# Kernel optimization log

Measured on AMD Instinct MI355X. Metric: run time of the kernel, lower is better.

Reference implementation:

```python
import jax, jax.numpy as jnp
import numpy as np

B, N, DIM = 4, 2048, 1024
HEADS, DIM_HEAD = 16, 64
SCALE = DIM_HEAD ** -0.5


def setup_inputs() -> dict:
    key = jax.random.key(0)
    ks = jax.random.split(key, 5)
    x = jax.random.normal(ks[0], (B, N, DIM), dtype=jnp.float32)
    s = DIM ** -0.5
    Wq = jax.random.normal(ks[1], (DIM, HEADS * DIM_HEAD), dtype=jnp.float32) * s
    Wk = jax.random.normal(ks[2], (DIM, HEADS * DIM_HEAD), dtype=jnp.float32) * s
    Wv = jax.random.normal(ks[3], (DIM, HEADS * DIM_HEAD), dtype=jnp.float32) * s
    Wo = jax.random.normal(ks[4], (HEADS * DIM_HEAD, DIM), dtype=jnp.float32) * s
    bo = jnp.zeros((DIM,), dtype=jnp.float32)
    return {"x": x, "Wq": Wq, "Wk": Wk, "Wv": Wv, "Wo": Wo, "bo": bo}


def reference(x, Wq, Wk, Wv, Wo, bo):
    b, n, _ = x.shape
    # project and split heads: [b, n, h, d] -> [b, h, n, d]
    def split_heads(t):
        return t.reshape(b, n, HEADS, DIM_HEAD).transpose(0, 2, 1, 3)
    q = split_heads(x @ Wq)
    k = split_heads(x @ Wk)
    v = split_heads(x @ Wv)
    dots = jnp.einsum("bhid,bhjd->bhij", q, k) * SCALE  # [b,h,n,n]
    attn = jax.nn.softmax(dots, axis=-1)
    out = jnp.einsum("bhij,bhjd->bhid", attn, v)  # [b,h,n,d]
    out = out.transpose(0, 2, 1, 3).reshape(b, n, HEADS * DIM_HEAD)
    # project_out is True (heads != 1); dropout is identity at inference
    return out @ Wo + bo
```

## Files before the change

kernel.cpp:

```cpp
#include <hip/hip_runtime.h>
#include <stdint.h>

typedef __attribute__((ext_vector_type(8))) short short8;
typedef __attribute__((ext_vector_type(8))) unsigned short u16x8;
typedef __attribute__((ext_vector_type(4))) float f32x4;

#define DEV static __device__ __forceinline__

DEV unsigned short f2bf(float f) {
  unsigned u = __builtin_bit_cast(unsigned, f);
  u += 0x7FFF + ((u >> 16) & 1);
  return (unsigned short)(u >> 16);
}

DEV unsigned cvtpk_bf16(float lo, float hi) {
  unsigned r;
  asm("v_cvt_pk_bf16_f32 %0, %1, %2" : "=v"(r) : "v"(lo), "v"(hi));
  return r;
}

#define GLOAD16(gptr, lptr)                                                        \
  __builtin_amdgcn_global_load_lds((const __attribute__((address_space(1))) void*)(gptr), \
                                   (__attribute__((address_space(3))) void*)(lptr), 16, 0, 0)

__global__ __launch_bounds__(256) void k_cast_x(const float* __restrict__ in,
                                                unsigned short* __restrict__ out) {
  int idx = (blockIdx.x * 256 + threadIdx.x) * 8;
  float4 a = *(const float4*)(in + idx);
  float4 b = *(const float4*)(in + idx + 4);
  u16x8 v;
  v[0] = f2bf(a.x); v[1] = f2bf(a.y); v[2] = f2bf(a.z); v[3] = f2bf(a.w);
  v[4] = f2bf(b.x); v[5] = f2bf(b.y); v[6] = f2bf(b.z); v[7] = f2bf(b.w);
  *(u16x8*)(out + idx) = v;
}

__global__ __launch_bounds__(256) void k_transW(const float* __restrict__ wq,
                                                const float* __restrict__ wk,
                                                const float* __restrict__ wv,
                                                const float* __restrict__ wo,
                                                unsigned short* __restrict__ wqkvT,
                                                unsigned short* __restrict__ woT) {
  __shared__ __align__(16) unsigned short t[64 * 72];
  int z = blockIdx.z;
  const float* src = (z == 0) ? wq : (z == 1) ? wk : (z == 2) ? wv : wo;
  unsigned short* dst = (z < 3) ? (wqkvT + (size_t)z * 1048576) : woT;
  int r0 = blockIdx.y * 64;
  int c0 = blockIdx.x * 64;
  int tid = threadIdx.x;
#pragma unroll
  for (int it = 0; it < 4; ++it) {
    int idx = it * 256 + tid;
    int il = idx >> 4;
    int c4 = idx & 15;
    float4 v = *(const float4*)(src + (size_t)(r0 + il) * 1024 + c0 + c4 * 4);
    t[(c4 * 4 + 0) * 72 + il] = f2bf(v.x);
    t[(c4 * 4 + 1) * 72 + il] = f2bf(v.y);
    t[(c4 * 4 + 2) * 72 + il] = f2bf(v.z);
    t[(c4 * 4 + 3) * 72 + il] = f2bf(v.w);
  }
  __syncthreads();
#pragma unroll
  for (int it = 0; it < 2; ++it) {
    int idx = it * 256 + tid;
    int ol = idx >> 3;
    int ch = idx & 7;
    *(u16x8*)(dst + (size_t)(c0 + ol) * 1024 + r0 + ch * 8) =
        *(const u16x8*)(t + ol * 72 + ch * 8);
  }
}

template <int MODE>
__global__ __launch_bounds__(256) void k_gemm(const unsigned short* __restrict__ A,
                                              const unsigned short* __restrict__ Bt,
                                              unsigned short* __restrict__ outB,
                                              unsigned short* __restrict__ vTout,
                                              float* __restrict__ outF,
                                              const float* __restrict__ bias) {
  __shared__ __align__(16) unsigned short sA[128 * 64];
  __shared__ __align__(16) unsigned short sB[128 * 64];
  const int tid = threadIdx.x;
  const int l = tid & 63;
  const int w = tid >> 6;
  const int m0 = blockIdx.y * 128;
  const int n0 = blockIdx.x * 128;
  const int wm = (w >> 1) * 64;
  const int wn = (w & 1) * 64;
  const int q16 = l & 15, g4 = l >> 4;
  const int lrow = l >> 3;
  const int lsw = ((l & 7) ^ lrow) * 8;

  const int z = blockIdx.z;
  const unsigned short* bt = Bt + (size_t)z * 1048576;
  unsigned short* dst = outB + (size_t)z * 8388608;
  const float sc = (MODE == 0 && z == 0) ? 0.125f * 1.44269504088896f : 1.0f;

  f32x4 acc[4][4];
#pragma unroll
  for (int i = 0; i < 4; ++i)
#pragma unroll
    for (int j = 0; j < 4; ++j) acc[i][j] = (f32x4){0.f, 0.f, 0.f, 0.f};

  for (int k0 = 0; k0 < 1024; k0 += 64) {
    __syncthreads();
#pragma unroll
    for (int r = 0; r < 4; ++r) {
      int chunk = w * 4 + r;
      int row = chunk * 8 + lrow;
      GLOAD16(A + (size_t)(m0 + row) * 1024 + k0 + lsw, sA + chunk * 512);
      GLOAD16(bt + (size_t)(n0 + row) * 1024 + k0 + lsw, sB + chunk * 512);
    }
    __syncthreads();
#pragma unroll
    for (int kk = 0; kk < 2; ++kk) {
      short8 af[4], bf_[4];
#pragma unroll
      for (int i = 0; i < 4; ++i) {
        int ra = wm + i * 16 + q16;
        af[i] = *(const short8*)(sA + ra * 64 + (((kk * 4 + g4) ^ (ra & 7)) * 8));
        int rb = wn + i * 16 + q16;
        bf_[i] = *(const short8*)(sB + rb * 64 + (((kk * 4 + g4) ^ (rb & 7)) * 8));
      }
#pragma unroll
      for (int mi = 0; mi < 4; ++mi)
#pragma unroll
        for (int ni = 0; ni < 4; ++ni)
          acc[mi][ni] =
              __builtin_amdgcn_mfma_f32_16x16x32_bf16(af[mi], bf_[ni], acc[mi][ni], 0, 0, 0);
    }
  }

  if (MODE == 0 && z == 2) {
#pragma unroll
    for (int mi = 0; mi < 4; ++mi) {
#pragma unroll
      for (int ni = 0; ni < 4; ++ni) {
        int row0 = m0 + wm + mi * 16 + g4 * 4;
        int col = n0 + wn + ni * 16 + q16;
        int b = row0 >> 11, seq0 = row0 & 2047;
        int h = col >> 6, d = col & 63;
        uint2 pv;
        pv.x = cvtpk_bf16(acc[mi][ni][0], acc[mi][ni][1]);
        pv.y = cvtpk_bf16(acc[mi][ni][2], acc[mi][ni][3]);
        *(uint2*)(vTout + (((size_t)(b * 16 + h) * 64 + d) * 2048 + seq0)) = pv;
      }
    }
  } else {
#pragma unroll
    for (int mi = 0; mi < 4; ++mi) {
#pragma unroll
      for (int ni = 0; ni < 4; ++ni) {
#pragma unroll
        for (int j = 0; j < 4; ++j) {
          int row = m0 + wm + mi * 16 + g4 * 4 + j;
          int col = n0 + wn + ni * 16 + q16;
          float val = acc[mi][ni][j];
          if (MODE == 0) {
            val *= sc;
            int b = row >> 11, seq = row & 2047;
            int h = col >> 6, d = col & 63;
            dst[((((size_t)b * 16 + h) * 2048 + seq) << 6) + d] = f2bf(val);
          } else {
            outF[(size_t)row * 1024 + col] = val + bias[col];
          }
        }
      }
    }
  }
}

__global__ __launch_bounds__(512) void k_attn(const unsigned short* __restrict__ Q,
                                              const unsigned short* __restrict__ Kg,
                                              const unsigned short* __restrict__ Vt,
                                              unsigned short* __restrict__ Oo) {
  __shared__ __align__(16) unsigned short sK[4][64 * 64];
  __shared__ __align__(16) unsigned short sV[4][64 * 64];
  __shared__ __align__(16) unsigned short sP[8][16 * 64];
  const int tid = threadIdx.x;
  const int l = tid & 63, w = tid >> 6;
  const int q16 = l & 15, g = l >> 4;
  const int bh = blockIdx.y;
  const int q0 = blockIdx.x * 128 + w * 16;
  const int lrow = l >> 3;
  const int lsw = ((l & 7) ^ lrow) * 8;

  const unsigned short* Qb = Q + ((size_t)bh * 2048 + q0) * 64;
  const unsigned short* Kb = Kg + (size_t)bh * 2048 * 64;
  const unsigned short* Vb = Vt + (size_t)bh * 64 * 2048;

  short8 qf[2];
#pragma unroll
  for (int s = 0; s < 2; ++s) qf[s] = *(const short8*)(Qb + q16 * 64 + s * 32 + g * 8);

  float sum = 0.f;
  f32x4 o[4];
#pragma unroll
  for (int dt = 0; dt < 4; ++dt) o[dt] = (f32x4){0.f, 0.f, 0.f, 0.f};

  auto STAGE = [&](int slot, int kv) {
    int row = w * 8 + lrow;
    GLOAD16(Kb + (size_t)(kv + row) * 64 + lsw, &sK[slot][w * 512]);
    GLOAD16(Vb + (size_t)row * 2048 + kv + lsw, &sV[slot][w * 512]);
  };

  auto COMPUTE = [&](int slot) {
    f32x4 st[4];
    __builtin_amdgcn_s_setprio(1);
#pragma unroll
    for (int t = 0; t < 4; ++t) {
      st[t] = (f32x4){0.f, 0.f, 0.f, 0.f};
#pragma unroll
      for (int s = 0; s < 2; ++s) {
        int key = t * 16 + q16;
        short8 kf = *(const short8*)(&sK[slot][key * 64 + (((s * 4 + g) ^ (key & 7)) * 8)]);
        st[t] = __builtin_amdgcn_mfma_f32_16x16x32_bf16(kf, qf[s], st[t], 0, 0, 0);
      }
    }
    __builtin_amdgcn_s_setprio(0);

    float p[4][4];
    float ps = 0.f;
#pragma unroll
    for (int t = 0; t < 4; ++t)
#pragma unroll
      for (int j = 0; j < 4; ++j) {
        p[t][j] = __builtin_amdgcn_exp2f(st[t][j]);
        ps += p[t][j];
      }
    ps += __shfl_xor(ps, 16);
    ps += __shfl_xor(ps, 32);
    sum += ps;

#pragma unroll
    for (int t = 0; t < 4; ++t) {
      uint2 pv;
      pv.x = cvtpk_bf16(p[t][0], p[t][1]);
      pv.y = cvtpk_bf16(p[t][2], p[t][3]);
      int c16 = t * 2 + (g >> 1);
      *(uint2*)(&sP[w][q16 * 64 + ((c16 ^ (q16 & 7)) * 8) + (g & 1) * 4]) = pv;
    }
    asm volatile("s_waitcnt lgkmcnt(0)" ::: "memory");
    __builtin_amdgcn_sched_barrier(0);

    __builtin_amdgcn_s_setprio(1);
#pragma unroll
    for (int win = 0; win < 2; ++win) {
      short8 pf = *(const short8*)(&sP[w][q16 * 64 + (((win * 4 + g) ^ (q16 & 7)) * 8)]);
#pragma unroll
      for (int dt = 0; dt < 4; ++dt) {
        int d = dt * 16 + q16;
        short8 vf = *(const short8*)(&sV[slot][d * 64 + (((win * 4 + g) ^ (d & 7)) * 8)]);
        o[dt] = __builtin_amdgcn_mfma_f32_16x16x32_bf16(pf, vf, o[dt], 0, 0, 0);
      }
    }
    __builtin_amdgcn_s_setprio(0);
  };

  STAGE(0, 0);
  STAGE(1, 64);
  asm volatile("s_waitcnt vmcnt(0)" ::: "memory");
  __syncthreads();

  for (int i = 0; i < 16; ++i) {
    const int sb = (i & 1) * 2;
    if (i < 15) {
      STAGE(sb ^ 2, (2 * i + 2) * 64);
      STAGE((sb ^ 2) + 1, (2 * i + 3) * 64);
    }
    COMPUTE(sb);
    COMPUTE(sb + 1);
    asm volatile("s_waitcnt vmcnt(0)" ::: "memory");
    __syncthreads();
  }

  float inv = 1.0f / sum;
  int b = bh >> 4, h = bh & 15;
#pragma unroll
  for (int j = 0; j < 4; ++j) {
    float ij = __shfl(inv, g * 4 + j);
#pragma unroll
    for (int dt = 0; dt < 4; ++dt)
      sP[w][(g * 4 + j) * 64 + dt * 16 + q16] = f2bf(o[dt][j] * ij);
  }
  unsigned short* Ob = Oo + ((size_t)b * 2048 + q0) * 1024 + h * 64;
#pragma unroll
  for (int it = 0; it < 2; ++it) {
    int flat = it * 512 + l * 8;
    int r = flat >> 6, c = flat & 63;
    *(u16x8*)(Ob + (size_t)r * 1024 + c) = *(const u16x8*)(&sP[w][r * 64 + c]);
  }
}

extern "C" void kernel_launch(void* const* d_in, const int* in_sizes, int n_in,
                              void* d_out, int out_size, void* d_ws, size_t ws_size,
                              hipStream_t stream) {
  const float* x = (const float*)d_in[0];
  const float* Wq = (const float*)d_in[1];
  const float* Wk = (const float*)d_in[2];
  const float* Wv = (const float*)d_in[3];
  const float* Wo = (const float*)d_in[4];
  const float* bo = (const float*)d_in[5];
  float* out = (float*)d_out;
  char* ws = (char*)d_ws;

  unsigned short* xb    = (unsigned short*)(ws);
  unsigned short* wqkvT = (unsigned short*)(ws + 16777216);
  unsigned short* woT   = (unsigned short*)(ws + 23068672);
  unsigned short* qkv   = (unsigned short*)(ws + 25165824);
  unsigned short* vT    = (unsigned short*)(ws + 75497472);
  unsigned short* aout  = xb;

  k_cast_x<<<4096, 256, 0, stream>>>(x, xb);
  k_transW<<<dim3(16, 16, 4), 256, 0, stream>>>(Wq, Wk, Wv, Wo, wqkvT, woT);
  k_gemm<0><<<dim3(8, 64, 3), 256, 0, stream>>>(xb, wqkvT, qkv, vT, nullptr, nullptr);
  k_attn<<<dim3(16, 64), 512, 0, stream>>>(qkv, qkv + 8388608, vT, aout);
  k_gemm<1><<<dim3(8, 64, 1), 256, 0, stream>>>(aout, woT, nullptr, nullptr, out, bo);
}
```

Baseline: 209.9 us.

## Rewrite QKV projection GEMM with 256x256 tiles, double-buffered LDS, and block swizzle

Replaces the templated QKV GEMM with a dedicated kernel that uses 512 threads and 256x256 output tiles. It double-buffers LDS so the next K-slice's global-to-LDS loads overlap the current MFMAs, raises wave priority around the MFMA block, and remaps the block index so neighbouring blocks share A/B tiles in cache. The larger tile cuts global reloads per FLOP. In exchange, 128 accumulators per thread raise register pressure and lower occupancy, and there are only 384 blocks to fill the GPU. The output GEMM is split into its own simplified kernel.

```diff
diff --git a/kernel.cpp b/kernel.cpp
--- a/kernel.cpp
+++ b/kernel.cpp
@@ -69,13 +69,112 @@
   }
 }
 
-template <int MODE>
-__global__ __launch_bounds__(256) void k_gemm(const unsigned short* __restrict__ A,
-                                              const unsigned short* __restrict__ Bt,
-                                              unsigned short* __restrict__ outB,
-                                              unsigned short* __restrict__ vTout,
-                                              float* __restrict__ outF,
-                                              const float* __restrict__ bias) {
+__global__ __launch_bounds__(512) void k_qkv(const unsigned short* __restrict__ A,
+                                             const unsigned short* __restrict__ Bt,
+                                             unsigned short* __restrict__ outQK,
+                                             unsigned short* __restrict__ vTout) {
+  __shared__ __align__(16) unsigned short sA[2][256 * 64];
+  __shared__ __align__(16) unsigned short sB[2][256 * 64];
+  const int tid = threadIdx.x;
+  const int l = tid & 63, w = tid >> 6;
+  const int wr = w >> 2, wc = w & 3;
+  const int q16 = l & 15, g4 = l >> 4;
+  const int lrow = l >> 3;
+  const int lsw = ((l & 7) ^ lrow) * 8;
+
+  const int bid = blockIdx.x;
+  const int swz = (bid & 7) * 48 + (bid >> 3);
+  const int n0 = (swz % 12) * 256;
+  const int m0 = (swz / 12) * 256;
+  const int z = n0 >> 10;
+  const float sc = (z == 0) ? 0.125f * 1.44269504088896f : 1.0f;
+
+  f32x4 acc[8][4];
+#pragma unroll
+  for (int i = 0; i < 8; ++i)
+#pragma unroll
+    for (int j = 0; j < 4; ++j) acc[i][j] = (f32x4){0.f, 0.f, 0.f, 0.f};
+
+#pragma unroll
+  for (int p = 0; p < 4; ++p) {
+    int chunk = w * 4 + p, row = chunk * 8 + lrow;
+    GLOAD16(A + (size_t)(m0 + row) * 1024 + lsw, &sA[0][chunk * 512]);
+    GLOAD16(Bt + (size_t)(n0 + row) * 1024 + lsw, &sB[0][chunk * 512]);
+  }
+
+  for (int t = 0; t < 16; ++t) {
+    const int buf = t & 1, nxt = buf ^ 1;
+    const int k1 = (t + 1) * 64;
+    asm volatile("s_waitcnt vmcnt(0)" ::: "memory");
+    __builtin_amdgcn_s_barrier();
+#pragma unroll
+    for (int p = 0; p < 4; ++p) {
+      if (t < 15) {
+        int chunk = w * 4 + p, row = chunk * 8 + lrow;
+        GLOAD16(A + (size_t)(m0 + row) * 1024 + k1 + lsw, &sA[nxt][chunk * 512]);
+        GLOAD16(Bt + (size_t)(n0 + row) * 1024 + k1 + lsw, &sB[nxt][chunk * 512]);
+      }
+      if (p) __builtin_amdgcn_s_barrier();
+      const int s = p & 1, mh = p >> 1;
+      short8 af[4], bfr[4];
+#pragma unroll
+      for (int i = 0; i < 4; ++i) {
+        int ra = wr * 128 + (mh * 4 + i) * 16 + q16;
+        af[i] = *(const short8*)(&sA[buf][ra * 64 + (((s * 4 + g4) ^ (ra & 7)) * 8)]);
+        int rb = wc * 64 + i * 16 + q16;
+        bfr[i] = *(const short8*)(&sB[buf][rb * 64 + (((s * 4 + g4) ^ (rb & 7)) * 8)]);
+      }
+      asm volatile("s_waitcnt lgkmcnt(0)" ::: "memory");
+      __builtin_amdgcn_sched_barrier(0);
+      __builtin_amdgcn_s_setprio(1);
+#pragma unroll
+      for (int i = 0; i < 4; ++i)
+#pragma unroll
+        for (int n = 0; n < 4; ++n)
+          acc[mh * 4 + i][n] =
+              __builtin_amdgcn_mfma_f32_16x16x32_bf16(af[i], bfr[n], acc[mh * 4 + i][n], 0, 0, 0);
+      __builtin_amdgcn_s_setprio(0);
+    }
+  }
+
+  if (z == 2) {
+#pragma unroll
+    for (int mi = 0; mi < 8; ++mi) {
+#pragma unroll
+      for (int ni = 0; ni < 4; ++ni) {
+        int row0 = m0 + wr * 128 + mi * 16 + g4 * 4;
+        int col = (n0 & 1023) + wc * 64 + ni * 16 + q16;
+        int b = row0 >> 11, seq0 = row0 & 2047;
+        int h = col >> 6, d = col & 63;
+        uint2 pv;
+        pv.x = cvtpk_bf16(acc[mi][ni][0], acc[mi][ni][1]);
+        pv.y = cvtpk_bf16(acc[mi][ni][2], acc[mi][ni][3]);
+        *(uint2*)(vTout + (((size_t)(b * 16 + h) * 64 + d) * 2048 + seq0)) = pv;
+      }
+    }
+  } else {
+    unsigned short* dst = outQK + (size_t)z * 8388608;
+#pragma unroll
+    for (int mi = 0; mi < 8; ++mi) {
+#pragma unroll
+      for (int ni = 0; ni < 4; ++ni) {
+#pragma unroll
+        for (int j = 0; j < 4; ++j) {
+          int row = m0 + wr * 128 + mi * 16 + g4 * 4 + j;
+          int col = (n0 & 1023) + wc * 64 + ni * 16 + q16;
+          int b = row >> 11, seq = row & 2047;
+          int h = col >> 6, d = col & 63;
+          dst[((((size_t)b * 16 + h) * 2048 + seq) << 6) + d] = f2bf(acc[mi][ni][j] * sc);
+        }
+      }
+    }
+  }
+}
+
+__global__ __launch_bounds__(256) void k_gemmO(const unsigned short* __restrict__ A,
+                                               const unsigned short* __restrict__ Bt,
+                                               float* __restrict__ outF,
+                                               const float* __restrict__ bias) {
   __shared__ __align__(16) unsigned short sA[128 * 64];
   __shared__ __align__(16) unsigned short sB[128 * 64];
   const int tid = threadIdx.x;
@@ -89,11 +188,6 @@
   const int lrow = l >> 3;
   const int lsw = ((l & 7) ^ lrow) * 8;
 
-  const int z = blockIdx.z;
-  const unsigned short* bt = Bt + (size_t)z * 1048576;
-  unsigned short* dst = outB + (size_t)z * 8388608;
-  const float sc = (MODE == 0 && z == 0) ? 0.125f * 1.44269504088896f : 1.0f;
-
   f32x4 acc[4][4];
 #pragma unroll
   for (int i = 0; i < 4; ++i)
@@ -107,7 +201,7 @@
       int chunk = w * 4 + r;
       int row = chunk * 8 + lrow;
       GLOAD16(A + (size_t)(m0 + row) * 1024 + k0 + lsw, sA + chunk * 512);
-      GLOAD16(bt + (size_t)(n0 + row) * 1024 + k0 + lsw, sB + chunk * 512);
+      GLOAD16(Bt + (size_t)(n0 + row) * 1024 + k0 + lsw, sB + chunk * 512);
     }
     __syncthreads();
 #pragma unroll
@@ -129,40 +223,15 @@
     }
   }
 
-  if (MODE == 0 && z == 2) {
-#pragma unroll
-    for (int mi = 0; mi < 4; ++mi) {
-#pragma unroll
-      for (int ni = 0; ni < 4; ++ni) {
-        int row0 = m0 + wm + mi * 16 + g4 * 4;
+#pragma unroll
+  for (int mi = 0; mi < 4; ++mi) {
+#pragma unroll
+    for (int ni = 0; ni < 4; ++ni) {
+#pragma unroll
+      for (int j = 0; j < 4; ++j) {
+        int row = m0 + wm + mi * 16 + g4 * 4 + j;
         int col = n0 + wn + ni * 16 + q16;
-        int b = row0 >> 11, seq0 = row0 & 2047;
-        int h = col >> 6, d = col & 63;
-        uint2 pv;
-        pv.x = cvtpk_bf16(acc[mi][ni][0], acc[mi][ni][1]);
-        pv.y = cvtpk_bf16(acc[mi][ni][2], acc[mi][ni][3]);
-        *(uint2*)(vTout + (((size_t)(b * 16 + h) * 64 + d) * 2048 + seq0)) = pv;
-      }
-    }
-  } else {
-#pragma unroll
-    for (int mi = 0; mi < 4; ++mi) {
-#pragma unroll
-      for (int ni = 0; ni < 4; ++ni) {
-#pragma unroll
-        for (int j = 0; j < 4; ++j) {
-          int row = m0 + wm + mi * 16 + g4 * 4 + j;
-          int col = n0 + wn + ni * 16 + q16;
-          float val = acc[mi][ni][j];
-          if (MODE == 0) {
-            val *= sc;
-            int b = row >> 11, seq = row & 2047;
-            int h = col >> 6, d = col & 63;
-            dst[((((size_t)b * 16 + h) * 2048 + seq) << 6) + d] = f2bf(val);
-          } else {
-            outF[(size_t)row * 1024 + col] = val + bias[col];
-          }
-        }
+        outF[(size_t)row * 1024 + col] = acc[mi][ni][j] + bias[col];
       }
     }
   }
@@ -311,7 +380,7 @@
 
   k_cast_x<<<4096, 256, 0, stream>>>(x, xb);
   k_transW<<<dim3(16, 16, 4), 256, 0, stream>>>(Wq, Wk, Wv, Wo, wqkvT, woT);
-  k_gemm<0><<<dim3(8, 64, 3), 256, 0, stream>>>(xb, wqkvT, qkv, vT, nullptr, nullptr);
+  k_qkv<<<384, 512, 0, stream>>>(xb, wqkvT, qkv, vT);
   k_attn<<<dim3(16, 64), 512, 0, stream>>>(qkv, qkv + 8388608, vT, aout);
-  k_gemm<1><<<dim3(8, 64, 1), 256, 0, stream>>>(aout, woT, nullptr, nullptr, out, bo);
-}
+  k_gemmO<<<dim3(8, 64), 256, 0, stream>>>(aout, woT, out, bo);
+}
```

Result: slower. 215.0 us (+2.4%).
